# Performance work log

Measured on AMD Instinct MI355X. Metric: run time of the kernel, lower is better.

## Reference

```python
import jax, jax.numpy as jnp
import numpy as np

N, D, E, H, K = 16384, 256, 8, 512, 2


def setup_inputs() -> dict:
    key = jax.random.key(0)
    ks = jax.random.split(key, 5)
    inputs = jax.random.normal(ks[0], (N, D), dtype=jnp.float32)
    Wg = jax.random.normal(ks[1], (D, E), dtype=jnp.float32) * 0.05
    w1 = jax.random.normal(ks[2], (E, D, H), dtype=jnp.float32) * 0.05
    b1 = jnp.zeros((E, H), dtype=jnp.float32)
    w2 = jax.random.normal(ks[3], (E, H, D), dtype=jnp.float32) * 0.05
    b2 = jnp.zeros((E, D), dtype=jnp.float32)
    return {"inputs": inputs, "Wg": Wg, "w1": w1, "b1": b1, "w2": w2, "b2": b2}


def reference(inputs, Wg, w1, b1, w2, b2):
    # gate + top-k routing (softmax over the selected logits only, as in the torch code)
    gate_logits = inputs @ Wg                       # [N, E]
    topw, topi = jax.lax.top_k(gate_logits, K)      # [N, K]
    topw = jax.nn.softmax(topw.astype(jnp.float32), axis=1).astype(inputs.dtype)
    # combine weights scattered back into a dense [N, E] matrix (dispatch/combine)
    combine = jnp.zeros((N, E), dtype=inputs.dtype)
    combine = combine.at[jnp.arange(N)[:, None], topi].add(topw)  # [N, E]
    # expert MLP (Linear -> GELU(exact) -> Linear), computed per expert and
    # combined with the sparse routing weights (pool='sum')
    h = jax.nn.gelu(jnp.einsum('nd,edh->neh', inputs, w1) + b1[None], approximate=False)  # [N,E,H]
    y = jnp.einsum('neh,ehd->ned', h, w2) + b2[None]                                      # [N,E,D]
    return jnp.einsum('ne,ned->nd', combine, y)                                           # [N,D]
```

## Files before the change

### kernel.cpp

```cpp
#include <hip/hip_runtime.h>

#define NTOK 16384
#define DIM 256
#define NEXP 8
#define HID 512
#define CAP 5120
#define CSTRIDE 16
#define HC 32
#define A2S 40

typedef unsigned short ushort_t;
typedef short bf16x8 __attribute__((ext_vector_type(8)));
typedef float f32x4 __attribute__((ext_vector_type(4)));

static __device__ __forceinline__ ushort_t f2bf(float f) {
    unsigned int u = __float_as_uint(f);
    unsigned int r = (u + 0x7FFFu + ((u >> 16) & 1u)) >> 16;
    return (ushort_t)r;
}
static __device__ __forceinline__ float bf2f(ushort_t u) {
    unsigned int x = ((unsigned int)u) << 16;
    return __uint_as_float(x);
}
static __device__ __forceinline__ float gelu_fast(float v) {
    float v2 = v * v;
    float u = v * __builtin_fmaf(v2, -0.1029407079f, -2.3022090196f);
    float e = __builtin_amdgcn_exp2f(u);
    return v * __builtin_amdgcn_rcpf(1.0f + e);
}
#define PIN(x) asm volatile("" : "+v"(x))

__global__ void k_transpose(const float* __restrict__ w1, const float* __restrict__ w2,
                            ushort_t* __restrict__ w1t, ushort_t* __restrict__ w2t,
                            int* __restrict__ counts) {
    __shared__ ushort_t tile[64][72];
    if (blockIdx.x == 0 && threadIdx.x < NEXP * CSTRIDE) counts[threadIdx.x] = 0;
    int b = blockIdx.x;
    const float* src; ushort_t* dst; int R, C, e, t;
    if (b < 256) { e = b >> 5; t = b & 31; src = w1; dst = w1t + e * DIM * HID; R = DIM; C = HID; }
    else { b -= 256; e = b >> 5; t = b & 31; src = w2; dst = w2t + e * DIM * HID; R = HID; C = DIM; }
    size_t ebase = (size_t)e * DIM * HID;
    int tilesC = C >> 6;
    int rt = t / tilesC, ct = t % tilesC;
    for (int i = 0; i < 16; i++) {
        int flat = i * 256 + threadIdx.x;
        int lr = flat >> 6, lc = flat & 63;
        tile[lr][lc] = f2bf(src[ebase + (size_t)(rt * 64 + lr) * C + ct * 64 + lc]);
    }
    __syncthreads();
    for (int i = 0; i < 16; i++) {
        int flat = i * 256 + threadIdx.x;
        int lr = flat >> 6, lc = flat & 63;
        dst[(ct * 64 + lr) * R + rt * 64 + lc] = tile[lc][lr];
    }
}

__global__ void k_router(const float* __restrict__ X, const float* __restrict__ Wg,
                         int* counts, int* tok_list, int* inv_idx, float* inv_w,
                         ushort_t* __restrict__ Xb) {
    __shared__ float xs[64][257];
    __shared__ float lg[64][8];
    __shared__ int te0[64], te1[64], lo0[64], lo1[64];
    __shared__ float tw0[64], tw1[64];
    __shared__ int lcnt[NEXP], gbase[NEXP];
    int tid = threadIdx.x;
    int tok0 = blockIdx.x * 64;
    if (tid < NEXP) lcnt[tid] = 0;
    for (int i = 0; i < 8; i++) {
        int flat = i * 256 + tid;
        int r = flat >> 5, c8 = (flat & 31) << 3;
        const float* row = X + (size_t)(tok0 + r) * DIM + c8;
        float4 a = *(const float4*)row;
        float4 b = *(const float4*)(row + 4);
        xs[r][c8 + 0] = a.x; xs[r][c8 + 1] = a.y; xs[r][c8 + 2] = a.z; xs[r][c8 + 3] = a.w;
        xs[r][c8 + 4] = b.x; xs[r][c8 + 5] = b.y; xs[r][c8 + 6] = b.z; xs[r][c8 + 7] = b.w;
    }
    __syncthreads();
    for (int i = 0; i < 8; i++) {
        int flat = i * 256 + tid;
        int r = flat >> 5, c8 = (flat & 31) << 3;
        ushort_t pk[8];
#pragma unroll
        for (int j = 0; j < 8; j++) pk[j] = f2bf(xs[r][c8 + j]);
        *(int4*)(Xb + (size_t)(tok0 + r) * DIM + c8) = *(const int4*)pk;
    }
    int tl = tid & 63, pair = tid >> 6;
    float l0 = 0.f, l1 = 0.f;
    for (int d = 0; d < DIM; d++) {
        float x = xs[tl][d];
        l0 += x * Wg[d * NEXP + 2 * pair];
        l1 += x * Wg[d * NEXP + 2 * pair + 1];
    }
    lg[tl][2 * pair] = l0; lg[tl][2 * pair + 1] = l1;
    __syncthreads();
    if (tid < 64) {
        float best = -1e30f; int bi = 0;
#pragma unroll
        for (int e = 0; e < NEXP; e++) { float v = lg[tid][e]; if (v > best) { best = v; bi = e; } }
        float best2 = -1e30f; int bi2 = 0;
#pragma unroll
        for (int e = 0; e < NEXP; e++) { if (e == bi) continue; float v = lg[tid][e]; if (v > best2) { best2 = v; bi2 = e; } }
        float ed = __expf(best2 - best);
        te0[tid] = bi; te1[tid] = bi2;
        tw0[tid] = 1.0f / (1.0f + ed);
        tw1[tid] = ed / (1.0f + ed);
        lo0[tid] = atomicAdd(&lcnt[bi], 1);
        lo1[tid] = atomicAdd(&lcnt[bi2], 1);
    }
    __syncthreads();
    if (tid < NEXP) gbase[tid] = atomicAdd(&counts[tid * CSTRIDE], lcnt[tid]);
    __syncthreads();
    if (tid < 64) {
        int token = tok0 + tid;
        int e0 = te0[tid], e1 = te1[tid];
        int p0 = gbase[e0] + lo0[tid]; if (p0 >= CAP) p0 = CAP - 1;
        int p1 = gbase[e1] + lo1[tid]; if (p1 >= CAP) p1 = CAP - 1;
        tok_list[e0 * CAP + p0] = token;
        tok_list[e1 * CAP + p1] = token;
        inv_idx[token * 2]     = (e0 << 16) | p0;  inv_w[token * 2]     = tw0[tid];
        inv_idx[token * 2 + 1] = (e1 << 16) | p1;  inv_w[token * 2 + 1] = tw1[tid];
    }
}

__launch_bounds__(256, 3)
__global__ void k_mlp_fused(const ushort_t* __restrict__ Xb,
                            const ushort_t* __restrict__ w1t, const float* __restrict__ b1,
                            const ushort_t* __restrict__ w2t, const float* __restrict__ b2,
                            const int* __restrict__ counts, const int* __restrict__ tok_list,
                            ushort_t* __restrict__ yb) {
    __shared__ ushort_t A1[HC * 264];
    __shared__ ushort_t A2[DIM * A2S];
    __shared__ ushort_t HB[64 * A2S];
    int b = blockIdx.x;
    int e = b / 80;
    int tile = b % 80;
    int count = counts[e * CSTRIDE];
    if (count > CAP) count = CAP;
    int t0 = tile * 64;
    if (t0 >= count) return;

    int tid = threadIdx.x;
    int w = tid >> 6, l = tid & 63, ln = l & 15, q = l >> 4;

    int arow = t0 + 16 * w + ln;
    int ci = (arow < count) ? arow : (count - 1);
    int atok = tok_list[e * CAP + ci];
    const ushort_t* xrow = Xb + (size_t)atok * DIM;
    bf16x8 xf[8];
#pragma unroll
    for (int ks = 0; ks < 8; ks++)
        xf[ks] = *(const bf16x8*)(xrow + ks * 32 + q * 8);
#pragma unroll
    for (int ks = 0; ks < 8; ks++) PIN(xf[ks]);

    const ushort_t* w1te = w1t + (size_t)e * DIM * HID;
    const ushort_t* w2te = w2t + (size_t)e * DIM * HID;

    f32x4 zf = {0.f, 0.f, 0.f, 0.f};
    f32x4 yacc[16];
#pragma unroll
    for (int i = 0; i < 16; i++) yacc[i] = zf;

    for (int ic = 0; ic < 16; ic++) {
        int hc = ic * HC;
        __syncthreads();
#pragma unroll
        for (int i = 0; i < 4; i++) {
            int flat = i * 256 + tid;
            int hr = flat >> 5, c8 = (flat & 31) << 3;
            *(int4*)(A1 + hr * 264 + c8) = *(const int4*)(w1te + (size_t)(hc + hr) * DIM + c8);
        }
#pragma unroll
        for (int i = 0; i < 4; i++) {
            int flat = i * 256 + tid;
            int dr = flat >> 2, c8 = (flat & 3) << 3;
            *(int4*)(A2 + dr * A2S + c8) = *(const int4*)(w2te + (size_t)dr * HID + hc + c8);
        }
        __syncthreads();

        f32x4 hacc[2];
        hacc[0] = zf; hacc[1] = zf;
#pragma unroll
        for (int ks = 0; ks < 8; ks++) {
            bf16x8 xk = xf[ks];
#pragma unroll
            for (int cf = 0; cf < 2; cf++) {
                bf16x8 wfr = *(const bf16x8*)(A1 + (cf * 16 + ln) * 264 + ks * 32 + q * 8);
                hacc[cf] = __builtin_amdgcn_mfma_f32_16x16x32_bf16(wfr, xk, hacc[cf], 0, 0, 0);
            }
        }
#pragma unroll
        for (int cf = 0; cf < 2; cf++) {
            float4 bv = *(const float4*)(b1 + e * HID + hc + cf * 16 + q * 4);
            ushort4 pk;
            pk.x = f2bf(gelu_fast(hacc[cf][0] + bv.x));
            pk.y = f2bf(gelu_fast(hacc[cf][1] + bv.y));
            pk.z = f2bf(gelu_fast(hacc[cf][2] + bv.z));
            pk.w = f2bf(gelu_fast(hacc[cf][3] + bv.w));
            *(ushort4*)(HB + (16 * w + ln) * A2S + cf * 16 + q * 4) = pk;
        }
        bf16x8 hf = *(const bf16x8*)(HB + (16 * w + ln) * A2S + q * 8);
#pragma unroll
        for (int cf2 = 0; cf2 < 16; cf2++) {
            bf16x8 wfr2 = *(const bf16x8*)(A2 + (cf2 * 16 + ln) * A2S + q * 8);
            yacc[cf2] = __builtin_amdgcn_mfma_f32_16x16x32_bf16(wfr2, hf, yacc[cf2], 0, 0, 0);
        }
    }
    size_t yrowbase = ((size_t)e * CAP + arow) * DIM;
#pragma unroll
    for (int cf2 = 0; cf2 < 16; cf2++) {
        float4 bv = *(const float4*)(b2 + e * DIM + cf2 * 16 + q * 4);
        ushort4 pk;
        pk.x = f2bf(yacc[cf2][0] + bv.x);
        pk.y = f2bf(yacc[cf2][1] + bv.y);
        pk.z = f2bf(yacc[cf2][2] + bv.z);
        pk.w = f2bf(yacc[cf2][3] + bv.w);
        *(ushort4*)(yb + yrowbase + cf2 * 16 + q * 4) = pk;
    }
}

__global__ void k_combine(const ushort_t* __restrict__ yb, const int* __restrict__ inv_idx,
                          const float* __restrict__ inv_w, float* __restrict__ out) {
    int tid = threadIdx.x;
    int n = blockIdx.x * 8 + (tid >> 5);
    int l32 = tid & 31, c8 = l32 << 3;
    int i0 = inv_idx[2 * n], i1 = inv_idx[2 * n + 1];
    float w0 = inv_w[2 * n], w1 = inv_w[2 * n + 1];
    size_t r0 = (size_t)(i0 >> 16) * CAP + (i0 & 0xFFFF);
    size_t r1 = (size_t)(i1 >> 16) * CAP + (i1 & 0xFFFF);
    int4 v0 = *(const int4*)(yb + r0 * DIM + c8);
    int4 v1 = *(const int4*)(yb + r1 * DIM + c8);
    ushort_t* p0 = (ushort_t*)&v0;
    ushort_t* p1 = (ushort_t*)&v1;
    float4 oa, ob;
    oa.x = w0 * bf2f(p0[0]) + w1 * bf2f(p1[0]);
    oa.y = w0 * bf2f(p0[1]) + w1 * bf2f(p1[1]);
    oa.z = w0 * bf2f(p0[2]) + w1 * bf2f(p1[2]);
    oa.w = w0 * bf2f(p0[3]) + w1 * bf2f(p1[3]);
    ob.x = w0 * bf2f(p0[4]) + w1 * bf2f(p1[4]);
    ob.y = w0 * bf2f(p0[5]) + w1 * bf2f(p1[5]);
    ob.z = w0 * bf2f(p0[6]) + w1 * bf2f(p1[6]);
    ob.w = w0 * bf2f(p0[7]) + w1 * bf2f(p1[7]);
    float4* op = (float4*)(out + (size_t)n * DIM + c8);
    op[0] = oa; op[1] = ob;
}

extern "C" void kernel_launch(void* const* d_in, const int* in_sizes, int n_in,
                              void* d_out, int out_size, void* d_ws, size_t ws_size,
                              hipStream_t stream) {
    const float* X  = (const float*)d_in[0];
    const float* Wg = (const float*)d_in[1];
    const float* w1 = (const float*)d_in[2];
    const float* b1 = (const float*)d_in[3];
    const float* w2 = (const float*)d_in[4];
    const float* b2 = (const float*)d_in[5];

    char* ws = (char*)d_ws;
    size_t off = 0;
    int* counts = (int*)(ws + off);        off = 1024;
    int* tok_list = (int*)(ws + off);      off += (size_t)NEXP * CAP * 4;
    int* inv_idx = (int*)(ws + off);       off += (size_t)NTOK * 2 * 4;
    float* inv_w = (float*)(ws + off);     off += (size_t)NTOK * 2 * 4;
    ushort_t* w1t = (ushort_t*)(ws + off); off += (size_t)NEXP * DIM * HID * 2;
    ushort_t* w2t = (ushort_t*)(ws + off); off += (size_t)NEXP * DIM * HID * 2;
    ushort_t* Xb = (ushort_t*)(ws + off);  off += (size_t)NTOK * DIM * 2;
    ushort_t* yb = (ushort_t*)(ws + off);  off += (size_t)NEXP * CAP * DIM * 2;

    k_transpose<<<512, 256, 0, stream>>>(w1, w2, w1t, w2t, counts);
    k_router<<<256, 256, 0, stream>>>(X, Wg, counts, tok_list, inv_idx, inv_w, Xb);
    k_mlp_fused<<<NEXP * 80, 256, 0, stream>>>(Xb, w1t, b1, w2t, b2, counts, tok_list, yb);
    k_combine<<<2048, 256, 0, stream>>>(yb, inv_idx, inv_w, (float*)d_out);
}
```

Baseline: 153.4 us.

## Prefetch next weight chunk into registers and raise MFMA wave priority

Weight tiles for the next hidden chunk are now loaded from global memory into registers while the current chunk computes, then written to LDS at the top of the next iteration. The explicit __syncthreads pair becomes raw s_barrier calls with a manual lgkmcnt wait. MFMA sections are also wrapped in s_setprio to favour matrix work across waves. This aims to hide global load latency behind compute, at the cost of extra registers that may lower occupancy, and it relies on the hand-placed wait for correctness.

```diff
diff --git a/kernel.cpp b/kernel.cpp
--- a/kernel.cpp
+++ b/kernel.cpp
@@ -161,25 +161,41 @@
 #pragma unroll
     for (int i = 0; i < 16; i++) yacc[i] = zf;
 
+    int f1r = tid >> 5,  f1c = (tid & 31) << 3;
+    int f2r = tid >> 2,  f2c = (tid & 3) << 3;
+    int4 r1[4], r2[4];
+#pragma unroll
+    for (int i = 0; i < 4; i++)
+        r1[i] = *(const int4*)(w1te + (size_t)(0 + f1r + i * 8) * DIM + f1c);
+#pragma unroll
+    for (int i = 0; i < 4; i++)
+        r2[i] = *(const int4*)(w2te + (size_t)(f2r + i * 64) * HID + 0 + f2c);
+
     for (int ic = 0; ic < 16; ic++) {
         int hc = ic * HC;
-        __syncthreads();
-#pragma unroll
-        for (int i = 0; i < 4; i++) {
-            int flat = i * 256 + tid;
-            int hr = flat >> 5, c8 = (flat & 31) << 3;
-            *(int4*)(A1 + hr * 264 + c8) = *(const int4*)(w1te + (size_t)(hc + hr) * DIM + c8);
-        }
-#pragma unroll
-        for (int i = 0; i < 4; i++) {
-            int flat = i * 256 + tid;
-            int dr = flat >> 2, c8 = (flat & 3) << 3;
-            *(int4*)(A2 + dr * A2S + c8) = *(const int4*)(w2te + (size_t)dr * HID + hc + c8);
-        }
-        __syncthreads();
+        __builtin_amdgcn_s_barrier();
+#pragma unroll
+        for (int i = 0; i < 4; i++)
+            *(int4*)(A1 + (f1r + i * 8) * 264 + f1c) = r1[i];
+#pragma unroll
+        for (int i = 0; i < 4; i++)
+            *(int4*)(A2 + (f2r + i * 64) * A2S + f2c) = r2[i];
+        if (ic < 15) {
+            int hn = hc + HC;
+#pragma unroll
+            for (int i = 0; i < 4; i++)
+                r1[i] = *(const int4*)(w1te + (size_t)(hn + f1r + i * 8) * DIM + f1c);
+#pragma unroll
+            for (int i = 0; i < 4; i++)
+                r2[i] = *(const int4*)(w2te + (size_t)(f2r + i * 64) * HID + hn + f2c);
+        }
+        asm volatile("s_waitcnt lgkmcnt(0)" ::: "memory");
+        __builtin_amdgcn_sched_barrier(0);
+        __builtin_amdgcn_s_barrier();
 
         f32x4 hacc[2];
         hacc[0] = zf; hacc[1] = zf;
+        __builtin_amdgcn_s_setprio(1);
 #pragma unroll
         for (int ks = 0; ks < 8; ks++) {
             bf16x8 xk = xf[ks];
@@ -189,6 +205,7 @@
                 hacc[cf] = __builtin_amdgcn_mfma_f32_16x16x32_bf16(wfr, xk, hacc[cf], 0, 0, 0);
             }
         }
+        __builtin_amdgcn_s_setprio(0);
 #pragma unroll
         for (int cf = 0; cf < 2; cf++) {
             float4 bv = *(const float4*)(b1 + e * HID + hc + cf * 16 + q * 4);
@@ -200,11 +217,13 @@
             *(ushort4*)(HB + (16 * w + ln) * A2S + cf * 16 + q * 4) = pk;
         }
         bf16x8 hf = *(const bf16x8*)(HB + (16 * w + ln) * A2S + q * 8);
+        __builtin_amdgcn_s_setprio(1);
 #pragma unroll
         for (int cf2 = 0; cf2 < 16; cf2++) {
             bf16x8 wfr2 = *(const bf16x8*)(A2 + (cf2 * 16 + ln) * A2S + q * 8);
             yacc[cf2] = __builtin_amdgcn_mfma_f32_16x16x32_bf16(wfr2, hf, yacc[cf2], 0, 0, 0);
         }
+        __builtin_amdgcn_s_setprio(0);
     }
     size_t yrowbase = ((size_t)e * CAP + arow) * DIM;
 #pragma unroll
```

Measured after the change: 230.3 us. +50.1%, slower.

## Double-buffer expert weight tiles via direct global-to-LDS loads with XOR swizzle

Applied to the files above, without the earlier changes.

Replaces the synchronous register-staged copies of the w1 and w2 chunks into shared memory with `global_load_lds` DMA into two LDS buffers. The next hidden chunk is prefetched while MFMAs run on the current one, which removes one barrier per iteration. The padded layouts give way to XOR-swizzled row layouts to keep MFMA fragment reads free of bank conflicts. LDS use roughly doubles, so launch bounds drop from 3 to 2 blocks per CU, trading occupancy for overlap of load and compute.

```diff
diff --git a/kernel.cpp b/kernel.cpp
--- a/kernel.cpp
+++ b/kernel.cpp
@@ -12,6 +12,9 @@
 typedef unsigned short ushort_t;
 typedef short bf16x8 __attribute__((ext_vector_type(8)));
 typedef float f32x4 __attribute__((ext_vector_type(4)));
+
+#define ASG __attribute__((address_space(1)))
+#define ASL __attribute__((address_space(3)))
 
 static __device__ __forceinline__ ushort_t f2bf(float f) {
     unsigned int u = __float_as_uint(f);
@@ -122,14 +125,14 @@
     }
 }
 
-__launch_bounds__(256, 3)
+__launch_bounds__(256, 2)
 __global__ void k_mlp_fused(const ushort_t* __restrict__ Xb,
                             const ushort_t* __restrict__ w1t, const float* __restrict__ b1,
                             const ushort_t* __restrict__ w2t, const float* __restrict__ b2,
                             const int* __restrict__ counts, const int* __restrict__ tok_list,
                             ushort_t* __restrict__ yb) {
-    __shared__ ushort_t A1[HC * 264];
-    __shared__ ushort_t A2[DIM * A2S];
+    __shared__ ushort_t A1[2][HC * DIM];
+    __shared__ ushort_t A2[2][DIM * HC];
     __shared__ ushort_t HB[64 * A2S];
     int b = blockIdx.x;
     int e = b / 80;
@@ -161,22 +164,31 @@
 #pragma unroll
     for (int i = 0; i < 16; i++) yacc[i] = zf;
 
+#define STAGE(hcs, pb)                                                                   \
+    {                                                                                    \
+        _Pragma("unroll")                                                                \
+        for (int i = 0; i < 4; i++) {                                                    \
+            int g = w * 4 + i;                                                           \
+            int r1_ = (g << 1) + (l >> 5);                             \
+            int cb1_ = ((l & 31) << 4) ^ ((r1_ & 7) << 4);                               \
+            const char* s1_ = (const char*)(w1te + (size_t)((hcs) + r1_) * DIM) + cb1_;  \
+            __builtin_amdgcn_global_load_lds((ASG const void*)s1_,                       \
+                (ASL void*)((char*)&A1[pb][0] + (g << 10)), 16, 0, 0);                   \
+            int r2_ = (g << 4) + (l >> 2);                            \
+            int cb2_ = ((l & 3) << 4) ^ ((r2_ & 3) << 4);                                \
+            const char* s2_ = (const char*)(w2te + (size_t)r2_ * HID + (hcs)) + cb2_;    \
+            __builtin_amdgcn_global_load_lds((ASG const void*)s2_,                       \
+                (ASL void*)((char*)&A2[pb][0] + (g << 10)), 16, 0, 0);                   \
+        }                                                                                \
+    }
+
+    STAGE(0, 0);
+    __syncthreads();
+
     for (int ic = 0; ic < 16; ic++) {
         int hc = ic * HC;
-        __syncthreads();
-#pragma unroll
-        for (int i = 0; i < 4; i++) {
-            int flat = i * 256 + tid;
-            int hr = flat >> 5, c8 = (flat & 31) << 3;
-            *(int4*)(A1 + hr * 264 + c8) = *(const int4*)(w1te + (size_t)(hc + hr) * DIM + c8);
-        }
-#pragma unroll
-        for (int i = 0; i < 4; i++) {
-            int flat = i * 256 + tid;
-            int dr = flat >> 2, c8 = (flat & 3) << 3;
-            *(int4*)(A2 + dr * A2S + c8) = *(const int4*)(w2te + (size_t)dr * HID + hc + c8);
-        }
-        __syncthreads();
+        int p = ic & 1;
+        if (ic < 15) STAGE(hc + HC, p ^ 1);
 
         f32x4 hacc[2];
         hacc[0] = zf; hacc[1] = zf;
@@ -185,7 +197,8 @@
             bf16x8 xk = xf[ks];
 #pragma unroll
             for (int cf = 0; cf < 2; cf++) {
-                bf16x8 wfr = *(const bf16x8*)(A1 + (cf * 16 + ln) * 264 + ks * 32 + q * 8);
+                int row = cf * 16 + ln;
+                bf16x8 wfr = *(const bf16x8*)(&A1[p][row * DIM + (((ks * 4 + q) ^ (row & 7)) << 3)]);
                 hacc[cf] = __builtin_amdgcn_mfma_f32_16x16x32_bf16(wfr, xk, hacc[cf], 0, 0, 0);
             }
         }
@@ -202,9 +215,11 @@
         bf16x8 hf = *(const bf16x8*)(HB + (16 * w + ln) * A2S + q * 8);
 #pragma unroll
         for (int cf2 = 0; cf2 < 16; cf2++) {
-            bf16x8 wfr2 = *(const bf16x8*)(A2 + (cf2 * 16 + ln) * A2S + q * 8);
+            int row2 = cf2 * 16 + ln;
+            bf16x8 wfr2 = *(const bf16x8*)(&A2[p][row2 * HC + ((q ^ (row2 & 3)) << 3)]);
             yacc[cf2] = __builtin_amdgcn_mfma_f32_16x16x32_bf16(wfr2, hf, yacc[cf2], 0, 0, 0);
         }
+        __syncthreads();
     }
     size_t yrowbase = ((size_t)e * CAP + arow) * DIM;
 #pragma unroll
@@ -217,6 +232,7 @@
         pk.w = f2bf(yacc[cf2][3] + bv.w);
         *(ushort4*)(yb + yrowbase + cf2 * 16 + q * 4) = pk;
     }
+#undef STAGE
 }
 
 __global__ void k_combine(const ushort_t* __restrict__ yb, const int* __restrict__ inv_idx,
```

Result: slower. 163.3 us (+6.5%).
